# Kernel tuning notes

Measured on AMD Instinct MI355X. Metric: run time of the kernel, lower is better.

The kernel has to match this reference:

```python
import jax, jax.numpy as jnp
import numpy as np

B, N, ZDIM = 8, 2048, 128
NPOINTS = 32
BN_EPS = 1e-5


def setup_inputs() -> dict:
    key = jax.random.key(0)
    ks = iter(jax.random.split(key, 64))

    def w(shape, s=0.05):
        return jax.random.normal(next(ks), shape, jnp.float32) * s

    inp = {"x": jax.random.normal(next(ks), (B, N, 3), jnp.float32)}
    inp.update(dict(
        w1=w((128, 3)), b1=w((128,)),
        w2=w((128, 128)), b2=w((128,)),
        w3=w((256, 128)), b3=w((256,)),
        w4=w((512, 256)), b4=w((512,)),
        a1_wqk=w((32, 1)), a1_wt=w((128, 128)), a1_bt=w((128,)),
        a2_wqk=w((32, 1)), a2_wt=w((128, 128)), a2_bt=w((128,)),
        a3_wqk=w((64, 1)), a3_wt=w((256, 256)), a3_bt=w((256,)),
        a4_wqk=w((128, 1)), a4_wt=w((512, 512)), a4_bt=w((512,)),
        fc1m_w=w((256, 512)), fc1m_b=w((256,)),
        fc2m_w=w((128, 256)), fc2m_b=w((128,)),
        fc3m_w=w((ZDIM, 128)), fc3m_b=w((ZDIM,)),
        fc1v_w=w((256, 512)), fc1v_b=w((256,)),
        fc2v_w=w((128, 256)), fc2v_b=w((128,)),
        fc3v_w=w((1, 128)), fc3v_b=w((1,)),
    ))
    return inp


def bn_cn(h):
    # BatchNorm1d over [B, C, N] features (training-mode batch stats, affine=identity at init)
    m = h.mean(axis=(0, 2), keepdims=True)
    v = h.var(axis=(0, 2), keepdims=True)
    return (h - m) * jax.lax.rsqrt(v + BN_EPS)


def bn_f(h):
    # BatchNorm1d over [B, F]
    m = h.mean(axis=0, keepdims=True)
    v = h.var(axis=0, keepdims=True)
    return (h - m) * jax.lax.rsqrt(v + BN_EPS)


def conv1x1(h, w, b):
    # 1x1 Conv1d: [B,Cin,N] x [Cout,Cin] -> [B,Cout,N]
    return jnp.einsum('oc,bcn->bon', w, h) + b[None, :, None]


def angle_density(xyz):
    # xyz: [B,N,3]; 1 - cosine similarity between all point pairs (computed as GEMM,
    # never materializing the [B,N,N,3] expanded tensors of the torch code)
    xn = xyz / jnp.linalg.norm(xyz, axis=-1, keepdims=True)
    dist = 1.0 - jnp.einsum('bnc,bmc->bnm', xn, xn)  # [B,N,N]
    neg_vals, _ = jax.lax.top_k(-dist, NPOINTS)       # 32 smallest distances
    feat_density = (-neg_vals).mean(axis=-1)          # [B,N]
    inv = 1.0 / feat_density
    return inv / jnp.max(inv)


def density_attn(h, dens, wqk, wt, bt):
    # h: [B,C,N], dens: [B,1,N]; q_conv and k_conv share weights
    q = jnp.einsum('dc,bcn->bdn', wqk, dens)          # [B,D4,N]
    energy = jnp.einsum('bdn,bdm->bnm', q, q)         # [B,N,N]
    attn = jax.nn.softmax(energy, axis=-1)
    attn = attn / (1e-9 + attn.sum(axis=1, keepdims=True))
    x_r = jnp.einsum('bcn,bnm->bcm', h, attn)         # [B,C,N]
    t = conv1x1(h - x_r, wt, bt)
    t = jax.nn.relu(bn_cn(t))
    return h + t


def reference(x, w1, b1, w2, b2, w3, b3, w4, b4,
              a1_wqk, a1_wt, a1_bt, a2_wqk, a2_wt, a2_bt,
              a3_wqk, a3_wt, a3_bt, a4_wqk, a4_wt, a4_bt,
              fc1m_w, fc1m_b, fc2m_w, fc2m_b, fc3m_w, fc3m_b,
              fc1v_w, fc1v_b, fc2v_w, fc2v_b, fc3v_w, fc3v_b):
    dens = angle_density(x)[:, None, :]               # [B,1,N]
    h = jnp.swapaxes(x, 1, 2)                         # [B,3,N]
    h = jax.nn.relu(bn_cn(conv1x1(h, w1, b1)))
    h = density_attn(h, dens, a1_wqk, a1_wt, a1_bt)
    h = jax.nn.relu(bn_cn(conv1x1(h, w2, b2)))
    h = density_attn(h, dens, a2_wqk, a2_wt, a2_bt)
    h = jax.nn.relu(bn_cn(conv1x1(h, w3, b3)))
    h = density_attn(h, dens, a3_wqk, a3_wt, a3_bt)
    h = bn_cn(conv1x1(h, w4, b4))                     # no relu on conv4 (matches source)
    h = density_attn(h, dens, a4_wqk, a4_wt, a4_bt)
    g = jnp.max(h, axis=2)                            # [B,512] global max pool

    u = jax.nn.relu(bn_f(g @ fc1m_w.T + fc1m_b))
    u = jax.nn.relu(bn_f(u @ fc2m_w.T + fc2m_b))
    u = u @ fc3m_w.T + fc3m_b
    u = u / jnp.linalg.norm(u, axis=-1, keepdims=True)

    k = jax.nn.relu(bn_f(g @ fc1v_w.T + fc1v_b))
    k = jax.nn.relu(bn_f(k @ fc2v_w.T + fc2v_b))
    k = k @ fc3v_w.T + fc3v_b
    k = jax.nn.softplus(k) + 1.0
    return (u, k)
```

## Files before the change

### kernel.cpp

```cpp
#include <hip/hip_runtime.h>
#include <cfloat>
#include <cmath>

constexpr int NB = 8;
constexpr int NP = 2048;
constexpr int NK = 11;

typedef __attribute__((ext_vector_type(4))) float f32x4;
typedef __attribute__((ext_vector_type(8))) short bf16x8;
#define MFMA16(a, b, c) __builtin_amdgcn_mfma_f32_16x16x32_bf16(a, b, c, 0, 0, 0)

__device__ inline ushort f2bf(float f) {
  union { float f; unsigned u; } v; v.f = f;
  unsigned r = v.u + 0x7FFFu + ((v.u >> 16) & 1u);
  return (ushort)(r >> 16);
}
__device__ inline unsigned pk2bf(float a, float b) {
  return (unsigned)f2bf(a) | ((unsigned)f2bf(b) << 16);
}

__device__ inline int dpp_half_sum_i32(int c) {
  c += __builtin_amdgcn_update_dpp(0, c, 0x111, 0xf, 0xf, true);
  c += __builtin_amdgcn_update_dpp(0, c, 0x112, 0xf, 0xf, true);
  c += __builtin_amdgcn_update_dpp(0, c, 0x114, 0xf, 0xf, true);
  c += __builtin_amdgcn_update_dpp(0, c, 0x118, 0xf, 0xf, true);
  c += __builtin_amdgcn_update_dpp(0, c, 0x142, 0xf, 0xf, true);
  return c;
}

__global__ void k_prep(const float* __restrict__ x, float* __restrict__ xn, float* __restrict__ xt) {
  int i = blockIdx.x * blockDim.x + threadIdx.x;
  if (i >= NB * NP) return;
  int b = i >> 11, n = i & (NP - 1);
  float a0 = x[i * 3 + 0], a1 = x[i * 3 + 1], a2 = x[i * 3 + 2];
  float rn = rsqrtf(a0 * a0 + a1 * a1 + a2 * a2);
  xn[i * 3 + 0] = a0 * rn; xn[i * 3 + 1] = a1 * rn; xn[i * 3 + 2] = a2 * rn;
  float* xb = xt + (size_t)b * 3 * NP;
  xb[0 * NP + n] = a0; xb[1 * NP + n] = a1; xb[2 * NP + n] = a2;
}

__global__ void k_zero1(float* p) { if (threadIdx.x == 0) p[0] = 0.f; }

__global__ __launch_bounds__(512, 1) void k_density(const float* __restrict__ xn,
                                                    float* __restrict__ inv,
                                                    int* __restrict__ maxinv) {
  __shared__ float sx[NP], sy[NP], sz[NP];
  int t = threadIdx.x;
  int w = t >> 6, lane = t & 63, half = lane >> 5, sl = lane & 31;
  int row0 = blockIdx.x * 16;
  int b = row0 >> 11;
  const float4* xb4 = (const float4*)(xn + (size_t)b * NP * 3);
  {
    float4 a = xb4[t * 3 + 0], c4 = xb4[t * 3 + 1], e4 = xb4[t * 3 + 2];
    int p = t * 4;
    sx[p + 0] = a.x;  sy[p + 0] = a.y;  sz[p + 0] = a.z;
    sx[p + 1] = a.w;  sy[p + 1] = c4.x; sz[p + 1] = c4.y;
    sx[p + 2] = c4.z; sy[p + 2] = c4.w; sz[p + 2] = e4.x;
    sx[p + 3] = e4.y; sy[p + 3] = e4.z; sz[p + 3] = e4.w;
  }
  __syncthreads();
  int row = row0 + w * 2 + half;
  int n = row & (NP - 1);
  float px = sx[n], py = sy[n], pz = sz[n];
  float d[64];
  float mn = FLT_MAX, mx = -FLT_MAX;
  #pragma unroll
  for (int k = 0; k < 64; ++k) {
    int m = sl + (k << 5);
    float v = 1.0f - (px * sx[m] + py * sy[m] + pz * sz[m]);
    d[k] = v;
    mn = fminf(mn, v); mx = fmaxf(mx, v);
  }
  #pragma unroll
  for (int off = 16; off; off >>= 1) {
    mn = fminf(mn, __shfl_xor(mn, off));
    mx = fminf(mx, __shfl_xor(mx, off));
  }
  float lo = mn, hi = mx + 1e-6f;
  int baddr = (half ? 63 : 31) << 2;
  for (int it = 0; it < 18; ++it) {
    float tt = 0.5f * (lo + hi);
    int c = 0;
    #pragma unroll
    for (int k = 0; k < 64; ++k) c += (d[k] < tt) ? 1 : 0;
    c = dpp_half_sum_i32(c);
    int ct = __builtin_amdgcn_ds_bpermute(baddr, c);
    bool le = ct <= 32;
    lo = le ? tt : lo;
    hi = le ? hi : tt;
  }
  float s = 0.f; int c = 0;
  #pragma unroll
  for (int k = 0; k < 64; ++k) {
    bool p = d[k] < lo;
    s += p ? d[k] : 0.f;
    c += p ? 1 : 0;
  }
  c = dpp_half_sum_i32(c);
  int ctot = __builtin_amdgcn_ds_bpermute(baddr, c);
  #pragma unroll
  for (int off = 16; off; off >>= 1) s += __shfl_xor(s, off);
  float sum = s + (float)(32 - ctot) * lo;
  if (sl == 0) {
    float iv = 32.0f / sum;
    inv[row] = iv;
    atomicMax(maxinv, __float_as_int(iv));
  }
}

__global__ void k_scale(float* __restrict__ dens, const float* __restrict__ maxinv) {
  int i = blockIdx.x * 256 + threadIdx.x;
  if (i < NB * NP) dens[i] *= (1.0f / maxinv[0]);
}

__global__ __launch_bounds__(64) void k_coef(const float* __restrict__ wqk, int D,
                                             float* __restrict__ coef) {
  int lane = threadIdx.x;
  float v = 0.f;
  for (int i = lane; i < D; i += 64) v += wqk[i] * wqk[i];
  #pragma unroll
  for (int off = 32; off; off >>= 1) v += __shfl_xor(v, off);
  if (lane == 0) {
    float c = 1.f;
    coef[0] = 1.f;
    for (int k = 1; k < NK; ++k) { c *= v / (float)k; coef[k] = c; }
  }
}

__global__ __launch_bounds__(256) void k_attn_small(const float* __restrict__ dens,
                                                    const float* __restrict__ coef,
                                                    float* __restrict__ rinv,
                                                    float* __restrict__ cinv) {
  int b = blockIdx.x, t = threadIdx.x, w = t >> 6, lane = t & 63;
  const float* db = dens + b * NP;
  float d[8], r[8];
  *(float4*)&d[0] = *(const float4*)(db + t * 8);
  *(float4*)&d[4] = *(const float4*)(db + t * 8 + 4);
  __shared__ float part[NK][4];
  float q[NK];
  {
    float acc[NK];
    #pragma unroll
    for (int k = 0; k < NK; ++k) acc[k] = 0.f;
    #pragma unroll
    for (int e = 0; e < 8; ++e) {
      float p = 1.f;
      #pragma unroll
      for (int k = 0; k < NK; ++k) { acc[k] += p; p *= d[e]; }
    }
    #pragma unroll
    for (int k = 0; k < NK; ++k) {
      float a = acc[k];
      #pragma unroll
      for (int off = 32; off; off >>= 1) a += __shfl_xor(a, off);
      if (lane == 0) part[k][w] = a;
    }
    __syncthreads();
    #pragma unroll
    for (int k = 0; k < NK; ++k)
      q[k] = coef[k] * ((part[k][0] + part[k][1]) + (part[k][2] + part[k][3]));
    __syncthreads();
  }
  #pragma unroll
  for (int e = 0; e < 8; ++e) {
    float poly = q[NK - 1];
    #pragma unroll
    for (int k = NK - 2; k >= 0; --k) poly = poly * d[e] + q[k];
    r[e] = 1.0f / poly;
  }
  *(float4*)(rinv + b * NP + t * 8)     = *(float4*)&r[0];
  *(float4*)(rinv + b * NP + t * 8 + 4) = *(float4*)&r[4];
  {
    float acc[NK];
    #pragma unroll
    for (int k = 0; k < NK; ++k) acc[k] = 0.f;
    #pragma unroll
    for (int e = 0; e < 8; ++e) {
      float p = r[e];
      #pragma unroll
      for (int k = 0; k < NK; ++k) { acc[k] += p; p *= d[e]; }
    }
    #pragma unroll
    for (int k = 0; k < NK; ++k) {
      float a = acc[k];
      #pragma unroll
      for (int off = 32; off; off >>= 1) a += __shfl_xor(a, off);
      if (lane == 0) part[k][w] = a;
    }
    __syncthreads();
    #pragma unroll
    for (int k = 0; k < NK; ++k)
      q[k] = coef[k] * ((part[k][0] + part[k][1]) + (part[k][2] + part[k][3]));
  }
  #pragma unroll
  for (int e = 0; e < 8; ++e) {
    float poly = q[NK - 1];
    #pragma unroll
    for (int k = NK - 2; k >= 0; --k) poly = poly * d[e] + q[k];
    r[e] = 1.0f / (poly + 1e-9f);
  }
  *(float4*)(cinv + b * NP + t * 8)     = *(float4*)&r[0];
  *(float4*)(cinv + b * NP + t * 8 + 4) = *(float4*)&r[4];
}

__global__ __launch_bounds__(256) void k_xrP(const float* __restrict__ H, float* __restrict__ U,
                                             const float* __restrict__ dens,
                                             const float* __restrict__ rinv,
                                             const float* __restrict__ cinv,
                                             const float* __restrict__ coef, int C) {
  int b = blockIdx.y, c = blockIdx.x, t = threadIdx.x, w = t >> 6, lane = t & 63;
  const float* Hc = H + ((size_t)b * C + c) * NP;
  float* Uc = U + ((size_t)b * C + c) * NP;
  const float* db = dens + b * NP;
  const float* rb = rinv + b * NP;
  const float* cb = cinv + b * NP;
  float h[8], d[8], r[8], cv[8];
  *(float4*)&h[0] = *(const float4*)(Hc + t * 8);
  *(float4*)&h[4] = *(const float4*)(Hc + t * 8 + 4);
  *(float4*)&d[0] = *(const float4*)(db + t * 8);
  *(float4*)&d[4] = *(const float4*)(db + t * 8 + 4);
  *(float4*)&r[0] = *(const float4*)(rb + t * 8);
  *(float4*)&r[4] = *(const float4*)(rb + t * 8 + 4);
  *(float4*)&cv[0] = *(const float4*)(cb + t * 8);
  *(float4*)&cv[4] = *(const float4*)(cb + t * 8 + 4);
  float acc[NK];
  #pragma unroll
  for (int k = 0; k < NK; ++k) acc[k] = 0.f;
  #pragma unroll
  for (int e = 0; e < 8; ++e) {
    float p = h[e] * r[e];
    #pragma unroll
    for (int k = 0; k < NK; ++k) { acc[k] += p; p *= d[e]; }
  }
  __shared__ float part[NK][4];
  #pragma unroll
  for (int k = 0; k < NK; ++k) {
    float a = acc[k];
    #pragma unroll
    for (int off = 32; off; off >>= 1) a += __shfl_xor(a, off);
    if (lane == 0) part[k][w] = a;
  }
  __syncthreads();
  float q[NK];
  #pragma unroll
  for (int k = 0; k < NK; ++k)
    q[k] = coef[k] * ((part[k][0] + part[k][1]) + (part[k][2] + part[k][3]));
  float u[8];
  #pragma unroll
  for (int e = 0; e < 8; ++e) {
    float poly = q[NK - 1];
    #pragma unroll
    for (int k = NK - 2; k >= 0; --k) poly = poly * d[e] + q[k];
    u[e] = h[e] - cv[e] * poly;
  }
  *(float4*)(Uc + t * 8)     = *(float4*)&u[0];
  *(float4*)(Uc + t * 8 + 4) = *(float4*)&u[4];
}

constexpr int LDA = 72;

__global__ __launch_bounds__(256) void k_gemm_mfma(const float* __restrict__ W,
                                                   const float* __restrict__ IN,
                                                   const float* __restrict__ bias,
                                                   float* __restrict__ OUT,
                                                   int Cin, int Cout) {
  int b = blockIdx.z, n0 = blockIdx.x * 128, o0 = blockIdx.y * 128;
  int tid = threadIdx.x, lane = tid & 63, w = tid >> 6;
  int wr = w >> 1, wc = w & 1;
  const float* Ib = IN + (size_t)b * Cin * NP;
  float* Ob = OUT + (size_t)b * Cout * NP;
  __shared__ ushort Asm[128 * LDA];
  __shared__ ushort Bsm[128 * LDA];
  f32x4 acc[4][4];
  #pragma unroll
  for (int i = 0; i < 4; ++i)
    #pragma unroll
    for (int j = 0; j < 4; ++j) acc[i][j] = (f32x4)(0.0f);

  int row = tid >> 1, half = tid & 1;
  int csub = tid & 63, q = tid >> 6;
  for (int cc0 = 0; cc0 < Cin; cc0 += 64) {
    __syncthreads();
    {
      const float* src = W + (size_t)(o0 + row) * Cin + cc0 + half * 32;
      unsigned* dst = (unsigned*)(Asm + row * LDA + half * 32);
      #pragma unroll
      for (int i = 0; i < 8; ++i) {
        float4 v = *(const float4*)(src + i * 4);
        dst[i * 2 + 0] = pk2bf(v.x, v.y);
        dst[i * 2 + 1] = pk2bf(v.z, v.w);
      }
      const float* isrc = Ib + (size_t)(cc0 + csub) * NP + n0 + q * 32;
      #pragma unroll
      for (int i = 0; i < 8; ++i) {
        float4 v = *(const float4*)(isrc + i * 4);
        ushort* bd = Bsm + (q * 32 + i * 4) * LDA + csub;
        bd[0]       = f2bf(v.x);
        bd[LDA]     = f2bf(v.y);
        bd[2 * LDA] = f2bf(v.z);
        bd[3 * LDA] = f2bf(v.w);
      }
    }
    __syncthreads();
    #pragma unroll
    for (int kk = 0; kk < 64; kk += 32) {
      bf16x8 af[4], bfr[4];
      #pragma unroll
      for (int i = 0; i < 4; ++i) {
        af[i]  = *(const bf16x8*)(Asm + (wr * 64 + i * 16 + (lane & 15)) * LDA + kk + (lane >> 4) * 8);
        bfr[i] = *(const bf16x8*)(Bsm + (wc * 64 + i * 16 + (lane & 15)) * LDA + kk + (lane >> 4) * 8);
      }
      #pragma unroll
      for (int i = 0; i < 4; ++i)
        #pragma unroll
        for (int j = 0; j < 4; ++j)
          acc[i][j] = MFMA16(af[i], bfr[j], acc[i][j]);
    }
  }
  #pragma unroll
  for (int i = 0; i < 4; ++i) {
    #pragma unroll
    for (int r = 0; r < 4; ++r) {
      int o = o0 + wr * 64 + i * 16 + (lane >> 4) * 4 + r;
      float bv = bias[o];
      #pragma unroll
      for (int j = 0; j < 4; ++j) {
        int n = n0 + wc * 64 + j * 16 + (lane & 15);
        Ob[(size_t)o * NP + n] = acc[i][j][r] + bv;
      }
    }
  }
}

__global__ __launch_bounds__(256) void k_gemm(const float* __restrict__ W,
                                              const float* __restrict__ IN,
                                              const float* __restrict__ bias,
                                              float* __restrict__ OUT,
                                              int Cin, int Cout) {
  int b = blockIdx.z;
  int n0 = blockIdx.x * 64;
  int o0 = blockIdx.y * 64;
  int tid = threadIdx.x;
  int tx = tid & 15, ty = tid >> 4;
  const float* Ib = IN + (size_t)b * Cin * NP;
  float* Ob = OUT + (size_t)b * Cout * NP;
  __shared__ float Wt[64][65];
  __shared__ float It[64][65];
  float acc[4][4] = {};
  for (int c0 = 0; c0 < Cin; c0 += 64) {
    __syncthreads();
    {
      int ci = tid & 63, ob4 = tid >> 6;
      bool cv = (c0 + ci) < Cin;
      #pragma unroll
      for (int k = 0; k < 16; ++k) {
        int oi = ob4 + (k << 2);
        Wt[ci][oi] = cv ? W[(size_t)(o0 + oi) * Cin + c0 + ci] : 0.f;
      }
      int ni = tid & 63, cb4 = tid >> 6;
      #pragma unroll
      for (int k = 0; k < 16; ++k) {
        int ci2 = cb4 + (k << 2);
        It[ci2][ni] = (c0 + ci2) < Cin ? Ib[(size_t)(c0 + ci2) * NP + n0 + ni] : 0.f;
      }
    }
    __syncthreads();
    #pragma unroll 4
    for (int ci = 0; ci < 64; ++ci) {
      float a0 = Wt[ci][ty * 4 + 0], a1 = Wt[ci][ty * 4 + 1], a2 = Wt[ci][ty * 4 + 2], a3 = Wt[ci][ty * 4 + 3];
      float b0 = It[ci][tx * 4 + 0], b1 = It[ci][tx * 4 + 1], b2 = It[ci][tx * 4 + 2], b3 = It[ci][tx * 4 + 3];
      acc[0][0] += a0 * b0; acc[0][1] += a0 * b1; acc[0][2] += a0 * b2; acc[0][3] += a0 * b3;
      acc[1][0] += a1 * b0; acc[1][1] += a1 * b1; acc[1][2] += a1 * b2; acc[1][3] += a1 * b3;
      acc[2][0] += a2 * b0; acc[2][1] += a2 * b1; acc[2][2] += a2 * b2; acc[2][3] += a2 * b3;
      acc[3][0] += a3 * b0; acc[3][1] += a3 * b1; acc[3][2] += a3 * b2; acc[3][3] += a3 * b3;
    }
  }
  #pragma unroll
  for (int i = 0; i < 4; ++i) {
    int o = o0 + ty * 4 + i;
    float bv = bias[o];
    #pragma unroll
    for (int j = 0; j < 4; ++j) {
      int n = n0 + tx * 4 + j;
      Ob[(size_t)o * NP + n] = acc[i][j] + bv;
    }
  }
}

__global__ __launch_bounds__(256) void k_bn(const float* __restrict__ T, float* __restrict__ H,
                                            int C, int relu, int acc) {
  int c = blockIdx.x, t = threadIdx.x, w = t >> 6, lane = t & 63;
  float4 v[16];
  float s = 0.f, s2 = 0.f;
  #pragma unroll
  for (int b = 0; b < NB; ++b) {
    const float4* p = (const float4*)(T + ((size_t)b * C + c) * NP);
    #pragma unroll
    for (int i = 0; i < 2; ++i) {
      float4 x = p[t + i * 256];
      v[b * 2 + i] = x;
      s += (x.x + x.y) + (x.z + x.w);
      s2 += (x.x * x.x + x.y * x.y) + (x.z * x.z + x.w * x.w);
    }
  }
  #pragma unroll
  for (int off = 32; off; off >>= 1) { s += __shfl_xor(s, off); s2 += __shfl_xor(s2, off); }
  __shared__ float ps[4], ps2[4];
  if (lane == 0) { ps[w] = s; ps2[w] = s2; }
  __syncthreads();
  float ts = (ps[0] + ps[1]) + (ps[2] + ps[3]);
  float ts2 = (ps2[0] + ps2[1]) + (ps2[2] + ps2[3]);
  float m = ts * (1.0f / (NB * NP));
  float var = ts2 * (1.0f / (NB * NP)) - m * m;
  float is = rsqrtf(var + 1e-5f);
  #pragma unroll
  for (int b = 0; b < NB; ++b) {
    float4* hp = (float4*)(H + ((size_t)b * C + c) * NP);
    #pragma unroll
    for (int i = 0; i < 2; ++i) {
      float4 x = v[b * 2 + i];
      x.x = (x.x - m) * is; x.y = (x.y - m) * is; x.z = (x.z - m) * is; x.w = (x.w - m) * is;
      if (relu) {
        x.x = fmaxf(x.x, 0.f); x.y = fmaxf(x.y, 0.f); x.z = fmaxf(x.z, 0.f); x.w = fmaxf(x.w, 0.f);
      }
      if (acc) {
        float4 h = hp[t + i * 256];
        x.x += h.x; x.y += h.y; x.z += h.z; x.w += h.w;
      }
      hp[t + i * 256] = x;
    }
  }
}

__global__ __launch_bounds__(64) void k_maxpool(const float* __restrict__ H, float* __restrict__ g) {
  int bf = blockIdx.x;
  const float* p = H + (size_t)bf * NP;
  int lane = threadIdx.x;
  float mx = -FLT_MAX;
  for (int n = lane; n < NP; n += 64) mx = fmaxf(mx, p[n]);
  #pragma unroll
  for (int off = 32; off > 0; off >>= 1) mx = fmaxf(mx, __shfl_xor(mx, off));
  if (lane == 0) g[bf] = mx;
}

__global__ __launch_bounds__(256) void k_head(const float* __restrict__ g,
    const float* __restrict__ f1mw, const float* __restrict__ f1mb,
    const float* __restrict__ f2mw, const float* __restrict__ f2mb,
    const float* __restrict__ f3mw, const float* __restrict__ f3mb,
    const float* __restrict__ f1vw, const float* __restrict__ f1vb,
    const float* __restrict__ f2vw, const float* __restrict__ f2vb,
    const float* __restrict__ f3vw, const float* __restrict__ f3vb,
    float* __restrict__ out) {
  bool vpath = (blockIdx.x == 1);
  const float* w1 = vpath ? f1vw : f1mw;
  const float* c1 = vpath ? f1vb : f1mb;
  const float* w2 = vpath ? f2vw : f2mw;
  const float* c2 = vpath ? f2vb : f2mb;
  __shared__ float gg[NB * 512];
  __shared__ float a1[NB * 256];
  __shared__ float a2[NB * 128];
  __shared__ float zz[NB * 128];
  __shared__ float nrm[NB];
  int t = threadIdx.x;
  for (int i = t; i < NB * 512; i += 256) gg[i] = g[i];
  __syncthreads();
  float o[NB];
  {
    #pragma unroll
    for (int b = 0; b < NB; ++b) o[b] = c1[t];
    const float* wr = w1 + (size_t)t * 512;
    for (int j = 0; j < 512; ++j) {
      float w = wr[j];
      #pragma unroll
      for (int b = 0; b < NB; ++b) o[b] += gg[b * 512 + j] * w;
    }
    float mean = 0.f;
    #pragma unroll
    for (int b = 0; b < NB; ++b) mean += o[b];
    mean *= (1.0f / NB);
    float var = 0.f;
    #pragma unroll
    for (int b = 0; b < NB; ++b) { float d = o[b] - mean; var += d * d; }
    var *= (1.0f / NB);
    float is = rsqrtf(var + 1e-5f);
    #pragma unroll
    for (int b = 0; b < NB; ++b) a1[b * 256 + t] = fmaxf((o[b] - mean) * is, 0.f);
  }
  __syncthreads();
  if (t < 128) {
    #pragma unroll
    for (int b = 0; b < NB; ++b) o[b] = c2[t];
    const float* wr = w2 + (size_t)t * 256;
    for (int j = 0; j < 256; ++j) {
      float w = wr[j];
      #pragma unroll
      for (int b = 0; b < NB; ++b) o[b] += a1[b * 256 + j] * w;
    }
    float mean = 0.f;
    #pragma unroll
    for (int b = 0; b < NB; ++b) mean += o[b];
    mean *= (1.0f / NB);
    float var = 0.f;
    #pragma unroll
    for (int b = 0; b < NB; ++b) { float d = o[b] - mean; var += d * d; }
    var *= (1.0f / NB);
    float is = rsqrtf(var + 1e-5f);
    #pragma unroll
    for (int b = 0; b < NB; ++b) a2[b * 128 + t] = fmaxf((o[b] - mean) * is, 0.f);
  }
  __syncthreads();
  if (!vpath) {
    if (t < 128) {
      const float* wr = f3mw + (size_t)t * 128;
      for (int b = 0; b < NB; ++b) {
        float s = f3mb[t];
        for (int j = 0; j < 128; ++j) s += a2[b * 128 + j] * wr[j];
        zz[b * 128 + t] = s;
      }
    }
    __syncthreads();
    if (t < NB) {
      float s = 0.f;
      for (int j = 0; j < 128; ++j) { float v = zz[t * 128 + j]; s += v * v; }
      nrm[t] = sqrtf(s);
    }
    __syncthreads();
    if (t < 128) {
      for (int b = 0; b < NB; ++b) out[b * 128 + t] = zz[b * 128 + t] / nrm[b];
    }
  } else {
    if (t < NB) {
      float s = f3vb[0];
      for (int j = 0; j < 128; ++j) s += a2[t * 128 + j] * f3vw[j];
      float sp = (s > 20.f) ? s : log1pf(expf(s));
      out[NB * 128 + t] = sp + 1.0f;
    }
  }
}

extern "C" void kernel_launch(void* const* d_in, const int* in_sizes, int n_in,
                              void* d_out, int out_size, void* d_ws, size_t ws_size,
                              hipStream_t stream) {
  const float* x  = (const float*)d_in[0];
  const float* w1 = (const float*)d_in[1];
  const float* b1 = (const float*)d_in[2];
  const float* w2 = (const float*)d_in[3];
  const float* b2 = (const float*)d_in[4];
  const float* w3 = (const float*)d_in[5];
  const float* b3 = (const float*)d_in[6];
  const float* w4 = (const float*)d_in[7];
  const float* b4 = (const float*)d_in[8];
  const float* a_wqk[4] = {(const float*)d_in[9],  (const float*)d_in[12], (const float*)d_in[15], (const float*)d_in[18]};
  const float* a_wt[4]  = {(const float*)d_in[10], (const float*)d_in[13], (const float*)d_in[16], (const float*)d_in[19]};
  const float* a_bt[4]  = {(const float*)d_in[11], (const float*)d_in[14], (const float*)d_in[17], (const float*)d_in[20]};
  int a_D[4] = {in_sizes[9], in_sizes[12], in_sizes[15], in_sizes[18]};
  const float* f1mw = (const float*)d_in[21]; const float* f1mb = (const float*)d_in[22];
  const float* f2mw = (const float*)d_in[23]; const float* f2mb = (const float*)d_in[24];
  const float* f3mw = (const float*)d_in[25]; const float* f3mb = (const float*)d_in[26];
  const float* f1vw = (const float*)d_in[27]; const float* f1vb = (const float*)d_in[28];
  const float* f2vw = (const float*)d_in[29]; const float* f2vb = (const float*)d_in[30];
  const float* f3vw = (const float*)d_in[31]; const float* f3vb = (const float*)d_in[32];
  float* out = (float*)d_out;

  float* ws = (float*)d_ws;
  float* xn     = ws; ws += (size_t)NB * NP * 3;
  float* dens   = ws; ws += NB * NP;
  float* maxinv = ws; ws += 16;
  float* coef   = ws; ws += 16;
  float* rinv   = ws; ws += NB * NP;
  float* cinv   = ws; ws += NB * NP;
  float* g      = ws; ws += NB * 512;
  float* Hb     = ws; ws += (size_t)NB * 512 * NP;
  float* Ub     = ws; ws += (size_t)NB * 512 * NP;
  float* Tb     = ws; ws += (size_t)NB * 512 * NP;

  k_prep<<<NB * NP / 256, 256, 0, stream>>>(x, xn, Ub);
  k_zero1<<<1, 64, 0, stream>>>(maxinv);
  k_density<<<NB * NP / 16, 512, 0, stream>>>(xn, dens, (int*)maxinv);
  k_scale<<<NB * NP / 256, 256, 0, stream>>>(dens, maxinv);

  auto conv = [&](const float* W, const float* bias, const float* IN, int Cin, int Cout, bool relu) {
    if (Cin < 64)
      k_gemm<<<dim3(NP / 64, Cout / 64, NB), 256, 0, stream>>>(W, IN, bias, Tb, Cin, Cout);
    else
      k_gemm_mfma<<<dim3(NP / 128, Cout / 128, NB), 256, 0, stream>>>(W, IN, bias, Tb, Cin, Cout);
    k_bn<<<Cout, 256, 0, stream>>>(Tb, Hb, Cout, relu ? 1 : 0, 0);
  };
  auto attn = [&](int li, int C) {
    k_coef<<<1, 64, 0, stream>>>(a_wqk[li], a_D[li], coef);
    k_attn_small<<<NB, 256, 0, stream>>>(dens, coef, rinv, cinv);
    k_xrP<<<dim3(C, NB), 256, 0, stream>>>(Hb, Ub, dens, rinv, cinv, coef, C);
    k_gemm_mfma<<<dim3(NP / 128, C / 128, NB), 256, 0, stream>>>(a_wt[li], Ub, a_bt[li], Tb, C, C);
    k_bn<<<C, 256, 0, stream>>>(Tb, Hb, C, 1, 1);
  };

  conv(w1, b1, Ub, 3, 128, true);
  attn(0, 128);
  conv(w2, b2, Hb, 128, 128, true);
  attn(1, 128);
  conv(w3, b3, Hb, 128, 256, true);
  attn(2, 256);
  conv(w4, b4, Hb, 256, 512, false);
  attn(3, 512);

  k_maxpool<<<NB * 512, 64, 0, stream>>>(Hb, g);
  k_head<<<2, 256, 0, stream>>>(g, f1mw, f1mb, f2mw, f2mb, f3mw, f3mb,
                                f1vw, f1vb, f2vw, f2vb, f3vw, f3vb, out);
}
```

Before: 478.4 us.

## Fuse max-pool into BN, fold coef into attn_small, use 4-way threshold search

```diff
diff --git a/kernel.cpp b/kernel.cpp
--- a/kernel.cpp
+++ b/kernel.cpp
@@ -78,16 +78,35 @@
   }
   float lo = mn, hi = mx + 1e-6f;
   int baddr = (half ? 63 : 31) << 2;
-  for (int it = 0; it < 18; ++it) {
+  for (int it = 0; it < 7; ++it) {
+    float dd = hi - lo;
+    float t1 = lo + 0.25f * dd, t2 = lo + 0.5f * dd, t3 = lo + 0.75f * dd;
+    int c12 = 0, c3 = 0;
+    #pragma unroll
+    for (int k = 0; k < 64; ++k) {
+      float v = d[k];
+      c12 += (v < t1 ? 1 : 0) + (v < t2 ? 65536 : 0);
+      c3  += (v < t3 ? 1 : 0);
+    }
+    c12 = dpp_half_sum_i32(c12);
+    c3  = dpp_half_sum_i32(c3);
+    c12 = __builtin_amdgcn_ds_bpermute(baddr, c12);
+    c3  = __builtin_amdgcn_ds_bpermute(baddr, c3);
+    int c1 = c12 & 0xFFFF, c2 = (int)(((unsigned)c12) >> 16);
+    bool le3 = c3 <= 32, le2 = c2 <= 32, le1 = c1 <= 32;
+    float nlo = le3 ? t3 : (le2 ? t2 : (le1 ? t1 : lo));
+    float nhi = le3 ? hi : (le2 ? t3 : (le1 ? t2 : t1));
+    lo = nlo; hi = nhi;
+  }
+  {
     float tt = 0.5f * (lo + hi);
     int c = 0;
     #pragma unroll
     for (int k = 0; k < 64; ++k) c += (d[k] < tt) ? 1 : 0;
     c = dpp_half_sum_i32(c);
-    int ct = __builtin_amdgcn_ds_bpermute(baddr, c);
-    bool le = ct <= 32;
+    c = __builtin_amdgcn_ds_bpermute(baddr, c);
+    bool le = c <= 32;
     lo = le ? tt : lo;
-    hi = le ? hi : tt;
   }
   float s = 0.f; int c = 0;
   #pragma unroll
@@ -113,25 +132,26 @@
   if (i < NB * NP) dens[i] *= (1.0f / maxinv[0]);
 }
 
-__global__ __launch_bounds__(64) void k_coef(const float* __restrict__ wqk, int D,
-                                             float* __restrict__ coef) {
-  int lane = threadIdx.x;
-  float v = 0.f;
-  for (int i = lane; i < D; i += 64) v += wqk[i] * wqk[i];
-  #pragma unroll
-  for (int off = 32; off; off >>= 1) v += __shfl_xor(v, off);
-  if (lane == 0) {
-    float c = 1.f;
-    coef[0] = 1.f;
-    for (int k = 1; k < NK; ++k) { c *= v / (float)k; coef[k] = c; }
-  }
-}
-
 __global__ __launch_bounds__(256) void k_attn_small(const float* __restrict__ dens,
-                                                    const float* __restrict__ coef,
+                                                    const float* __restrict__ wqk, int D,
+                                                    float* __restrict__ coef_out,
                                                     float* __restrict__ rinv,
                                                     float* __restrict__ cinv) {
   int b = blockIdx.x, t = threadIdx.x, w = t >> 6, lane = t & 63;
+  float sv = 0.f;
+  for (int i = lane; i < D; i += 64) sv += wqk[i] * wqk[i];
+  #pragma unroll
+  for (int off = 32; off; off >>= 1) sv += __shfl_xor(sv, off);
+  float coef[NK];
+  coef[0] = 1.f;
+  {
+    float cc = 1.f;
+    #pragma unroll
+    for (int k = 1; k < NK; ++k) { cc *= sv / (float)k; coef[k] = cc; }
+  }
+  if (b == 0 && t == 0) {
+    for (int k = 0; k < NK; ++k) coef_out[k] = coef[k];
+  }
   const float* db = dens + b * NP;
   float d[8], r[8];
   *(float4*)&d[0] = *(const float4*)(db + t * 8);
@@ -388,7 +408,8 @@
 }
 
 __global__ __launch_bounds__(256) void k_bn(const float* __restrict__ T, float* __restrict__ H,
-                                            int C, int relu, int acc) {
+                                            int C, int relu, int acc, int pool,
+                                            float* __restrict__ gout) {
   int c = blockIdx.x, t = threadIdx.x, w = t >> 6, lane = t & 63;
   float4 v[16];
   float s = 0.f, s2 = 0.f;
@@ -413,6 +434,9 @@
   float m = ts * (1.0f / (NB * NP));
   float var = ts2 * (1.0f / (NB * NP)) - m * m;
   float is = rsqrtf(var + 1e-5f);
+  float bmax[NB];
+  #pragma unroll
+  for (int b = 0; b < NB; ++b) bmax[b] = -FLT_MAX;
   #pragma unroll
   for (int b = 0; b < NB; ++b) {
     float4* hp = (float4*)(H + ((size_t)b * C + c) * NP);
@@ -428,19 +452,24 @@
         x.x += h.x; x.y += h.y; x.z += h.z; x.w += h.w;
       }
       hp[t + i * 256] = x;
-    }
-  }
-}
-
-__global__ __launch_bounds__(64) void k_maxpool(const float* __restrict__ H, float* __restrict__ g) {
-  int bf = blockIdx.x;
-  const float* p = H + (size_t)bf * NP;
-  int lane = threadIdx.x;
-  float mx = -FLT_MAX;
-  for (int n = lane; n < NP; n += 64) mx = fmaxf(mx, p[n]);
-  #pragma unroll
-  for (int off = 32; off > 0; off >>= 1) mx = fmaxf(mx, __shfl_xor(mx, off));
-  if (lane == 0) g[bf] = mx;
+      if (pool) bmax[b] = fmaxf(bmax[b], fmaxf(fmaxf(x.x, x.y), fmaxf(x.z, x.w)));
+    }
+  }
+  if (pool) {
+    __shared__ float pm[4][NB];
+    #pragma unroll
+    for (int b = 0; b < NB; ++b) {
+      float m2 = bmax[b];
+      #pragma unroll
+      for (int off = 32; off; off >>= 1) m2 = fmaxf(m2, __shfl_xor(m2, off));
+      if (lane == 0) pm[w][b] = m2;
+    }
+    __syncthreads();
+    if (t < NB) {
+      float m2 = fmaxf(fmaxf(pm[0][t], pm[1][t]), fmaxf(pm[2][t], pm[3][t]));
+      gout[t * C + c] = m2;
+    }
+  }
 }
 
 __global__ __launch_bounds__(256) void k_head(const float* __restrict__ g,
@@ -584,14 +613,13 @@
       k_gemm<<<dim3(NP / 64, Cout / 64, NB), 256, 0, stream>>>(W, IN, bias, Tb, Cin, Cout);
     else
       k_gemm_mfma<<<dim3(NP / 128, Cout / 128, NB), 256, 0, stream>>>(W, IN, bias, Tb, Cin, Cout);
-    k_bn<<<Cout, 256, 0, stream>>>(Tb, Hb, Cout, relu ? 1 : 0, 0);
+    k_bn<<<Cout, 256, 0, stream>>>(Tb, Hb, Cout, relu ? 1 : 0, 0, 0, g);
   };
   auto attn = [&](int li, int C) {
-    k_coef<<<1, 64, 0, stream>>>(a_wqk[li], a_D[li], coef);
-    k_attn_small<<<NB, 256, 0, stream>>>(dens, coef, rinv, cinv);
+    k_attn_small<<<NB, 256, 0, stream>>>(dens, a_wqk[li], a_D[li], coef, rinv, cinv);
     k_xrP<<<dim3(C, NB), 256, 0, stream>>>(Hb, Ub, dens, rinv, cinv, coef, C);
     k_gemm_mfma<<<dim3(NP / 128, C / 128, NB), 256, 0, stream>>>(a_wt[li], Ub, a_bt[li], Tb, C, C);
-    k_bn<<<C, 256, 0, stream>>>(Tb, Hb, C, 1, 1);
+    k_bn<<<C, 256, 0, stream>>>(Tb, Hb, C, 1, 1, (li == 3) ? 1 : 0, g);
   };
 
   conv(w1, b1, Ub, 3, 128, true);
@@ -603,7 +631,6 @@
   conv(w4, b4, Hb, 256, 512, false);
   attn(3, 512);
 
-  k_maxpool<<<NB * 512, 64, 0, stream>>>(Hb, g);
   k_head<<<2, 256, 0, stream>>>(g, f1mw, f1mb, f2mw, f2mb, f3mw, f3mb,
                                 f1vw, f1vb, f2vw, f2vb, f3vw, f3vb, out);
 }
```

Measured after the change: 467.8 us. 1.02x faster.
